# Kernel optimization log

Hardware: AMD Instinct MI355X
Metric: run time of the kernel (lower is better)

## Reference

```python
import jax, jax.numpy as jnp
import numpy as np

N = 50000
E = 1600000
D_IN, D_EMB, D_H, D_OUT, HEADS = 128, 128, 128, 64, 2


def setup_inputs() -> dict:
    key = jax.random.key(0)
    ks = jax.random.split(key, 12)
    return {
        "x": jax.random.normal(ks[0], (N, D_IN), jnp.float32),
        "edge_index": jax.random.randint(ks[1], (2, E), 0, N, dtype=jnp.int32),
        "node_indices": jnp.arange(N, dtype=jnp.int32),
        "emb": jax.random.normal(ks[2], (N, D_EMB), jnp.float32) * 0.1,
        "W_gcn": jax.random.normal(ks[3], (D_IN + D_EMB, D_H), jnp.float32) * 0.06,
        "b_gcn": jnp.zeros((D_H,), jnp.float32),
        "W_sage_l": jax.random.normal(ks[4], (D_H, D_H), jnp.float32) * 0.08,
        "W_sage_r": jax.random.normal(ks[5], (D_H, D_H), jnp.float32) * 0.08,
        "b_sage": jnp.zeros((D_H,), jnp.float32),
        "W_gat": jax.random.normal(ks[6], (D_H, HEADS, D_H), jnp.float32) * 0.08,
        "att_src": jax.random.normal(ks[7], (HEADS, D_H), jnp.float32) * 0.1,
        "att_dst": jax.random.normal(ks[8], (HEADS, D_H), jnp.float32) * 0.1,
        "b_gat": jnp.zeros((D_H,), jnp.float32),
        "W_out": jax.random.normal(ks[9], (D_H, D_OUT), jnp.float32) * 0.08,
        "b_out": jnp.zeros((D_OUT,), jnp.float32),
    }


def _forward(x, edge_index, node_indices, emb, W_gcn, b_gcn,
             W_sage_l, W_sage_r, b_sage, W_gat, att_src, att_dst, b_gat,
             W_out, b_out):
    n = x.shape[0]
    seg = jax.ops.segment_sum
    loops = jnp.arange(n, dtype=edge_index.dtype)

    # node2vec embedding lookup + concat
    h = jnp.concatenate([x, emb[node_indices]], axis=1)  # [N, D_IN+D_EMB]

    # --- GCNConv (symmetric norm, self loops) ---
    src = jnp.concatenate([edge_index[0], loops])
    dst = jnp.concatenate([edge_index[1], loops])
    deg = seg(jnp.ones_like(dst, jnp.float32), dst, num_segments=n)
    dinv = jnp.where(deg > 0, jax.lax.rsqrt(jnp.maximum(deg, 1.0)), 0.0)
    norm = dinv[src] * dinv[dst]                     # [E+N]
    hW = h @ W_gcn                                   # [N, D_H]
    h = seg(hW[src] * norm[:, None], dst, num_segments=n) + b_gcn
    h = jax.nn.relu(h)

    # --- SAGEConv (mean aggregation, no self loops) ---
    s, d = edge_index[0], edge_index[1]
    agg = seg(h[s], d, num_segments=n)
    cnt = seg(jnp.ones_like(d, jnp.float32), d, num_segments=n)
    mean = agg / jnp.maximum(cnt, 1.0)[:, None]
    h = mean @ W_sage_l + h @ W_sage_r + b_sage
    h = jax.nn.relu(h)

    # --- GATConv heads=2, concat=False (mean over heads), self loops ---
    xW = jnp.einsum('nd,dhc->nhc', h, W_gat)         # [N, H, D_H]
    a_src = jnp.einsum('nhc,hc->nh', xW, att_src)    # [N, H]
    a_dst = jnp.einsum('nhc,hc->nh', xW, att_dst)
    alpha = jax.nn.leaky_relu(a_src[src] + a_dst[dst], 0.2)  # [E+N, H]
    amax = jax.ops.segment_max(alpha, dst, num_segments=n)
    alpha = jnp.exp(alpha - amax[dst])
    asum = seg(alpha, dst, num_segments=n)
    alpha = alpha / (asum[dst] + 1e-16)
    out = seg(xW[src] * alpha[:, :, None], dst, num_segments=n)  # [N, H, D_H]
    h = jax.nn.relu(out.mean(axis=1) + b_gat)

    return h @ W_out + b_out


def reference(x, edge_index, node_indices, emb, W_gcn, b_gcn,
              W_sage_l, W_sage_r, b_sage, W_gat, att_src, att_dst, b_gat,
              W_out, b_out):
    return _forward(x, edge_index, node_indices, emb, W_gcn, b_gcn,
                    W_sage_l, W_sage_r, b_sage, W_gat, att_src, att_dst, b_gat,
                    W_out, b_out)
```

## Files before the change

### kernel.cpp

```cpp
#include <hip/hip_runtime.h>


typedef short bf16x8 __attribute__((ext_vector_type(8)));
typedef float f32x4  __attribute__((ext_vector_type(4)));

static __device__ __forceinline__ float leaky02(float x) {
    return x > 0.f ? x : 0.2f * x;
}
static __device__ __forceinline__ unsigned short f2bf(float f) {
    unsigned u = __float_as_uint(f);
    u = (u + 0x7FFFu + ((u >> 16) & 1u)) >> 16;
    return (unsigned short)u;
}
static __device__ __forceinline__ float bf2f(unsigned short h) {
    return __uint_as_float(((unsigned)h) << 16);
}
static __device__ __forceinline__ float4 bf4(ushort4 h) {
    return make_float4(bf2f(h.x), bf2f(h.y), bf2f(h.z), bf2f(h.w));
}
static __device__ __forceinline__ void split_bf(float v, unsigned short& h,
                                                unsigned short& l) {
    unsigned u = __float_as_uint(v);
    unsigned uh = u & 0xFFFF0000u;
    h = (unsigned short)(uh >> 16);
    l = f2bf(v - __uint_as_float(uh));
}

__global__ void deg_edges(const int* __restrict__ dst, int* __restrict__ degi, int E) {
    int e = blockIdx.x * blockDim.x + threadIdx.x;
    if (e < E) atomicAdd(&degi[dst[e]], 1);
}

__global__ __launch_bounds__(256)
void scan_part_norm(const int* __restrict__ degi, int* __restrict__ partial,
                    float* __restrict__ dinv, float* __restrict__ icnt, int n)
{
    int t = threadIdx.x;
    int base = blockIdx.x * 1024 + t * 4;
    int s = 0;
#pragma unroll
    for (int i = 0; i < 4; ++i) {
        int g = base + i;
        if (g < n) {
            int de = degi[g];
            s += de;
            dinv[g] = rsqrtf((float)(de + 1));
            icnt[g] = 1.0f / (float)(de > 1 ? de : 1);
        }
    }
#pragma unroll
    for (int m = 32; m > 0; m >>= 1) s += __shfl_xor(s, m, 64);
    __shared__ int wsum[4];
    if ((t & 63) == 0) wsum[t >> 6] = s;
    __syncthreads();
    if (t == 0) partial[blockIdx.x] = wsum[0] + wsum[1] + wsum[2] + wsum[3];
}

__global__ __launch_bounds__(64)
void scan_offsets(int* __restrict__ partial, int nb)
{
    int t = threadIdx.x;
    int carry = 0;
    for (int base = 0; base < nb; base += 64) {
        int i = base + t;
        int v = (i < nb) ? partial[i] : 0;
        int incl = v;
#pragma unroll
        for (int m = 1; m < 64; m <<= 1) {
            int o = __shfl_up(incl, m, 64);
            if (t >= m) incl += o;
        }
        if (i < nb) partial[i] = incl - v + carry;
        carry += __shfl(incl, 63, 64);
    }
}

__global__ __launch_bounds__(256)
void scan_write(const int* __restrict__ degi, const int* __restrict__ partial,
                int* __restrict__ rowptr, int n)
{
    __shared__ int tmp[256];
    int t = threadIdx.x;
    int base = blockIdx.x * 1024 + t * 4;
    int v[4]; int s = 0;
#pragma unroll
    for (int i = 0; i < 4; ++i) {
        int g = base + i;
        v[i] = (g < n) ? degi[g] : 0;
        s += v[i];
    }
    tmp[t] = s;
    __syncthreads();
    for (int off = 1; off < 256; off <<= 1) {
        int a = (t >= off) ? tmp[t - off] : 0;
        __syncthreads();
        tmp[t] += a;
        __syncthreads();
    }
    int run = tmp[t] - s + partial[blockIdx.x];
#pragma unroll
    for (int i = 0; i < 4; ++i) {
        int g = base + i;
        if (g < n) rowptr[g] = run;
        run += v[i];
    }
}

__global__ void csr_fill(const int* __restrict__ src, const int* __restrict__ dst,
                         int* __restrict__ rowptr, int* __restrict__ csr, int E)
{
    int e = blockIdx.x * blockDim.x + threadIdx.x;
    if (e >= E) return;
    int d = dst[e];
    int pos = atomicAdd(&rowptr[d], 1);
    csr[pos] = src[e];
}

static __device__ __forceinline__ void stage_w_split(
    const float* __restrict__ W, int ncW, int colOff, int kt, int t,
    unsigned short (*WBh)[65][8], unsigned short (*WBl)[65][8])
{
#pragma unroll
    for (int i = 0; i < 4; ++i) {
        int f = i * 256 + t;
        int wr = f >> 5, wc4 = (f & 31) << 2;
        float4 v = *(const float4*)(W + (size_t)(kt * 32 + wr) * ncW + colOff + wc4);
        int jj = wr & 7, kg16 = (wr >> 3) << 4;
        int nt = wc4 >> 4, sb = (wc4 & 15) + kg16;
        unsigned short h, l;
        split_bf(v.x, h, l); WBh[nt][sb + 0][jj] = h; WBl[nt][sb + 0][jj] = l;
        split_bf(v.y, h, l); WBh[nt][sb + 1][jj] = h; WBl[nt][sb + 1][jj] = l;
        split_bf(v.z, h, l); WBh[nt][sb + 2][jj] = h; WBl[nt][sb + 2][jj] = l;
        split_bf(v.w, h, l); WBh[nt][sb + 3][jj] = h; WBl[nt][sb + 3][jj] = l;
    }
}

__global__ __launch_bounds__(256)
void gemm_gcn(const float* __restrict__ A1, const float* __restrict__ W1,
              const float* __restrict__ A2, const float* __restrict__ W2,
              const int* __restrict__ idx2, const float* __restrict__ scale,
              unsigned short* __restrict__ C, int nrows)
{
    __shared__ unsigned short ABh[8][65][8];
    __shared__ unsigned short WBh[8][65][8], WBl[8][65][8];
    const int t    = threadIdx.x;
    const int lane = t & 63;
    const int wv   = t >> 6;
    const int l15  = lane & 15;
    const int lg   = lane >> 4;
    const int row0 = blockIdx.x * 128;

    f32x4 acc[2][8];
#pragma unroll
    for (int mt = 0; mt < 2; ++mt)
#pragma unroll
        for (int nt = 0; nt < 8; ++nt) acc[mt][nt] = (f32x4){0.f, 0.f, 0.f, 0.f};

    for (int p = 0; p < 2; ++p) {
        const float* A = (p == 0) ? A1 : A2;
        const float* W = (p == 0) ? W1 : W2;
        for (int kt = 0; kt < 4; ++kt) {
#pragma unroll
            for (int i = 0; i < 4; ++i) {
                int f = i * 256 + t;
                int r = f >> 3, c4 = (f & 7) << 2;
                int row = row0 + r; if (row >= nrows) row = nrows - 1;
                int arow = (p == 1) ? idx2[row] : row;
                float4 v = *(const float4*)(A + (size_t)arow * 128 + kt * 32 + c4);
                int slot = (r & 15) + ((c4 >> 3) << 4);
                *(ushort4*)&ABh[r >> 4][slot][c4 & 4] =
                    make_ushort4(f2bf(v.x), f2bf(v.y), f2bf(v.z), f2bf(v.w));
            }
            stage_w_split(W, 128, 0, kt, t, WBh, WBl);
            __syncthreads();
            bf16x8 a0 = *reinterpret_cast<const bf16x8*>(&ABh[wv * 2 + 0][lane][0]);
            bf16x8 a1 = *reinterpret_cast<const bf16x8*>(&ABh[wv * 2 + 1][lane][0]);
#pragma unroll
            for (int nt = 0; nt < 8; ++nt) {
                bf16x8 bh = *reinterpret_cast<const bf16x8*>(&WBh[nt][lane][0]);
                bf16x8 bl = *reinterpret_cast<const bf16x8*>(&WBl[nt][lane][0]);
                acc[0][nt] = __builtin_amdgcn_mfma_f32_16x16x32_bf16(a0, bl, acc[0][nt], 0, 0, 0);
                acc[0][nt] = __builtin_amdgcn_mfma_f32_16x16x32_bf16(a0, bh, acc[0][nt], 0, 0, 0);
                acc[1][nt] = __builtin_amdgcn_mfma_f32_16x16x32_bf16(a1, bl, acc[1][nt], 0, 0, 0);
                acc[1][nt] = __builtin_amdgcn_mfma_f32_16x16x32_bf16(a1, bh, acc[1][nt], 0, 0, 0);
            }
            __syncthreads();
        }
    }
#pragma unroll
    for (int mt = 0; mt < 2; ++mt) {
#pragma unroll
        for (int reg = 0; reg < 4; ++reg) {
            int row = row0 + wv * 32 + mt * 16 + lg * 4 + reg;
            if (row >= nrows) continue;
            float sc = scale[row];
            unsigned short* cp = C + (size_t)row * 128 + l15;
#pragma unroll
            for (int nt = 0; nt < 8; ++nt)
                cp[nt * 16] = f2bf(acc[mt][nt][reg] * sc);
        }
    }
}

__global__ __launch_bounds__(256)
void gemm_sage_gat(const unsigned short* __restrict__ meanb,
                   const float* __restrict__ W_sl,
                   const unsigned short* __restrict__ h1b,
                   const float* __restrict__ W_sr,
                   const float* __restrict__ b_sage,
                   const float* __restrict__ W_gat,
                   const float* __restrict__ att_src,
                   const float* __restrict__ att_dst,
                   float* __restrict__ a_s, float* __restrict__ a_d,
                   unsigned short* __restrict__ xWb, int nrows)
{
    __shared__ unsigned short ABh[8][65][8];
    __shared__ unsigned short WBh[8][65][8], WBl[8][65][8];
    __shared__ unsigned short H2[128][136];
    const int t    = threadIdx.x;
    const int lane = t & 63;
    const int wv   = t >> 6;
    const int l15  = lane & 15;
    const int lg   = lane >> 4;
    const int row0 = blockIdx.x * 128;

    f32x4 acc[2][8];
#pragma unroll
    for (int mt = 0; mt < 2; ++mt)
#pragma unroll
        for (int nt = 0; nt < 8; ++nt) acc[mt][nt] = (f32x4){0.f, 0.f, 0.f, 0.f};

    for (int p = 0; p < 2; ++p) {
        const unsigned short* A = (p == 0) ? meanb : h1b;
        const float* W = (p == 0) ? W_sl : W_sr;
        for (int kt = 0; kt < 4; ++kt) {
#pragma unroll
            for (int i = 0; i < 2; ++i) {
                int f = i * 256 + t;
                int r = f >> 2, kq = f & 3;
                int row = row0 + r; if (row >= nrows) row = nrows - 1;
                bf16x8 v = *(const bf16x8*)(A + (size_t)row * 128 + kt * 32 + kq * 8);
                *(bf16x8*)&ABh[r >> 4][(r & 15) + (kq << 4)][0] = v;
            }
            stage_w_split(W, 128, 0, kt, t, WBh, WBl);
            __syncthreads();
            bf16x8 a0 = *reinterpret_cast<const bf16x8*>(&ABh[wv * 2 + 0][lane][0]);
            bf16x8 a1 = *reinterpret_cast<const bf16x8*>(&ABh[wv * 2 + 1][lane][0]);
#pragma unroll
            for (int nt = 0; nt < 8; ++nt) {
                bf16x8 bh = *reinterpret_cast<const bf16x8*>(&WBh[nt][lane][0]);
                bf16x8 bl = *reinterpret_cast<const bf16x8*>(&WBl[nt][lane][0]);
                acc[0][nt] = __builtin_amdgcn_mfma_f32_16x16x32_bf16(a0, bl, acc[0][nt], 0, 0, 0);
                acc[0][nt] = __builtin_amdgcn_mfma_f32_16x16x32_bf16(a0, bh, acc[0][nt], 0, 0, 0);
                acc[1][nt] = __builtin_amdgcn_mfma_f32_16x16x32_bf16(a1, bl, acc[1][nt], 0, 0, 0);
                acc[1][nt] = __builtin_amdgcn_mfma_f32_16x16x32_bf16(a1, bh, acc[1][nt], 0, 0, 0);
            }
            __syncthreads();
        }
    }
    {
        float bias_v[8];
#pragma unroll
        for (int nt = 0; nt < 8; ++nt) bias_v[nt] = b_sage[nt * 16 + l15];
#pragma unroll
        for (int mt = 0; mt < 2; ++mt) {
#pragma unroll
            for (int reg = 0; reg < 4; ++reg) {
                int r = wv * 32 + mt * 16 + lg * 4 + reg;
#pragma unroll
                for (int nt = 0; nt < 8; ++nt) {
                    float v = fmaxf(acc[mt][nt][reg] + bias_v[nt], 0.f);
                    H2[r][nt * 16 + l15] = f2bf(v);
                }
            }
        }
    }
    __syncthreads();

    for (int ch = 0; ch < 2; ++ch) {
        f32x4 acc2[2][8];
#pragma unroll
        for (int mt = 0; mt < 2; ++mt)
#pragma unroll
            for (int nt = 0; nt < 8; ++nt) acc2[mt][nt] = (f32x4){0.f, 0.f, 0.f, 0.f};
        for (int kt = 0; kt < 4; ++kt) {
            stage_w_split(W_gat, 256, ch * 128, kt, t, WBh, WBl);
            __syncthreads();
            bf16x8 a0 = *(const bf16x8*)&H2[(wv * 2 + 0) * 16 + l15][kt * 32 + lg * 8];
            bf16x8 a1 = *(const bf16x8*)&H2[(wv * 2 + 1) * 16 + l15][kt * 32 + lg * 8];
#pragma unroll
            for (int nt = 0; nt < 8; ++nt) {
                bf16x8 bh = *reinterpret_cast<const bf16x8*>(&WBh[nt][lane][0]);
                bf16x8 bl = *reinterpret_cast<const bf16x8*>(&WBl[nt][lane][0]);
                acc2[0][nt] = __builtin_amdgcn_mfma_f32_16x16x32_bf16(a0, bl, acc2[0][nt], 0, 0, 0);
                acc2[0][nt] = __builtin_amdgcn_mfma_f32_16x16x32_bf16(a0, bh, acc2[0][nt], 0, 0, 0);
                acc2[1][nt] = __builtin_amdgcn_mfma_f32_16x16x32_bf16(a1, bl, acc2[1][nt], 0, 0, 0);
                acc2[1][nt] = __builtin_amdgcn_mfma_f32_16x16x32_bf16(a1, bh, acc2[1][nt], 0, 0, 0);
            }
            __syncthreads();
        }
        float as_v[8], ad_v[8];
#pragma unroll
        for (int nt = 0; nt < 8; ++nt) {
            int col = ch * 128 + nt * 16 + l15;
            as_v[nt] = att_src[col];
            ad_v[nt] = att_dst[col];
        }
#pragma unroll
        for (int mt = 0; mt < 2; ++mt) {
#pragma unroll
            for (int reg = 0; reg < 4; ++reg) {
                int row = row0 + wv * 32 + mt * 16 + lg * 4 + reg;
                bool ok = row < nrows;
                float ps = 0.f, pd = 0.f;
                unsigned short* cp =
                    xWb + (size_t)row * 256 + ch * 128 + l15;
#pragma unroll
                for (int nt = 0; nt < 8; ++nt) {
                    float v = acc2[mt][nt][reg];
                    if (ok) cp[nt * 16] = f2bf(v);
                    ps = fmaf(v, as_v[nt], ps);
                    pd = fmaf(v, ad_v[nt], pd);
                }
#pragma unroll
                for (int m = 1; m < 16; m <<= 1) {
                    ps += __shfl_xor(ps, m, 64);
                    pd += __shfl_xor(pd, m, 64);
                }
                if (ok && l15 == 0) {
                    a_s[row * 2 + ch] = ps;
                    a_d[row * 2 + ch] = pd;
                }
            }
        }
    }
}

__global__ __launch_bounds__(256)
void gcn_gather(const int* __restrict__ rowptr, const int* __restrict__ csr,
                const float* __restrict__ dinv,
                const unsigned short* __restrict__ hWb,
                const float* __restrict__ b,
                unsigned short* __restrict__ h1b, int n)
{
    int d = blockIdx.x * 4 + (threadIdx.x >> 6);
    if (d >= n) return;
    int lane = threadIdx.x & 63;
    int half = lane >> 5;
    int c = (lane & 31) << 2;
    int r1 = rowptr[d];
    int r0 = (d == 0) ? 0 : rowptr[d - 1];
    float4 acc = make_float4(0.f, 0.f, 0.f, 0.f);
    int j = r0 + half;
    for (; j + 6 < r1; j += 8) {
        int s0 = csr[j], s1 = csr[j + 2], s2 = csr[j + 4], s3 = csr[j + 6];
        float4 v0 = bf4(*(const ushort4*)(hWb + (size_t)s0 * 128 + c));
        float4 v1 = bf4(*(const ushort4*)(hWb + (size_t)s1 * 128 + c));
        float4 v2 = bf4(*(const ushort4*)(hWb + (size_t)s2 * 128 + c));
        float4 v3 = bf4(*(const ushort4*)(hWb + (size_t)s3 * 128 + c));
        acc.x += (v0.x + v1.x) + (v2.x + v3.x);
        acc.y += (v0.y + v1.y) + (v2.y + v3.y);
        acc.z += (v0.z + v1.z) + (v2.z + v3.z);
        acc.w += (v0.w + v1.w) + (v2.w + v3.w);
    }
    for (; j < r1; j += 2) {
        int s = csr[j];
        float4 v = bf4(*(const ushort4*)(hWb + (size_t)s * 128 + c));
        acc.x += v.x; acc.y += v.y; acc.z += v.z; acc.w += v.w;
    }
    acc.x += __shfl_xor(acc.x, 32, 64);
    acc.y += __shfl_xor(acc.y, 32, 64);
    acc.z += __shfl_xor(acc.z, 32, 64);
    acc.w += __shfl_xor(acc.w, 32, 64);
    if (lane < 32) {
        float dd = dinv[d];
        float4 vd = bf4(*(const ushort4*)(hWb + (size_t)d * 128 + c));
        float4 bb = *(const float4*)(b + c);
        float o0 = fmaxf(fmaf(acc.x + vd.x, dd, bb.x), 0.f);
        float o1 = fmaxf(fmaf(acc.y + vd.y, dd, bb.y), 0.f);
        float o2 = fmaxf(fmaf(acc.z + vd.z, dd, bb.z), 0.f);
        float o3 = fmaxf(fmaf(acc.w + vd.w, dd, bb.w), 0.f);
        *(ushort4*)(h1b + (size_t)d * 128 + c) =
            make_ushort4(f2bf(o0), f2bf(o1), f2bf(o2), f2bf(o3));
    }
}

__global__ __launch_bounds__(256)
void sage_gather(const int* __restrict__ rowptr, const int* __restrict__ csr,
                 const float* __restrict__ icnt,
                 const unsigned short* __restrict__ h1b,
                 unsigned short* __restrict__ meanb, int n)
{
    int d = blockIdx.x * 4 + (threadIdx.x >> 6);
    if (d >= n) return;
    int lane = threadIdx.x & 63;
    int half = lane >> 5;
    int c = (lane & 31) << 2;
    int r1 = rowptr[d];
    int r0 = (d == 0) ? 0 : rowptr[d - 1];
    float4 acc = make_float4(0.f, 0.f, 0.f, 0.f);
    int j = r0 + half;
    for (; j + 6 < r1; j += 8) {
        int s0 = csr[j], s1 = csr[j + 2], s2 = csr[j + 4], s3 = csr[j + 6];
        float4 v0 = bf4(*(const ushort4*)(h1b + (size_t)s0 * 128 + c));
        float4 v1 = bf4(*(const ushort4*)(h1b + (size_t)s1 * 128 + c));
        float4 v2 = bf4(*(const ushort4*)(h1b + (size_t)s2 * 128 + c));
        float4 v3 = bf4(*(const ushort4*)(h1b + (size_t)s3 * 128 + c));
        acc.x += (v0.x + v1.x) + (v2.x + v3.x);
        acc.y += (v0.y + v1.y) + (v2.y + v3.y);
        acc.z += (v0.z + v1.z) + (v2.z + v3.z);
        acc.w += (v0.w + v1.w) + (v2.w + v3.w);
    }
    for (; j < r1; j += 2) {
        int s = csr[j];
        float4 v = bf4(*(const ushort4*)(h1b + (size_t)s * 128 + c));
        acc.x += v.x; acc.y += v.y; acc.z += v.z; acc.w += v.w;
    }
    acc.x += __shfl_xor(acc.x, 32, 64);
    acc.y += __shfl_xor(acc.y, 32, 64);
    acc.z += __shfl_xor(acc.z, 32, 64);
    acc.w += __shfl_xor(acc.w, 32, 64);
    if (lane < 32) {
        float ic = icnt[d];
        *(ushort4*)(meanb + (size_t)d * 128 + c) =
            make_ushort4(f2bf(acc.x * ic), f2bf(acc.y * ic),
                         f2bf(acc.z * ic), f2bf(acc.w * ic));
    }
}

__global__ __launch_bounds__(256)
void gat_gather(const int* __restrict__ rowptr, const int* __restrict__ csr,
                const float* __restrict__ a_s, const float* __restrict__ a_d,
                const unsigned short* __restrict__ xWb,
                const float* __restrict__ b_gat,
                const float* __restrict__ W_out, const float* __restrict__ b_out,
                float* __restrict__ out, int n)
{
    __shared__ float h3row[4][128];
    int wv = threadIdx.x >> 6;
    int d = blockIdx.x * 4 + wv;
    if (d >= n) return;
    int lane = threadIdx.x & 63;
    const int hoff = lane >> 5;
    const int hsel = lane & 32;
    int r1 = rowptr[d];
    int r0 = (d == 0) ? 0 : rowptr[d - 1];
    const int nE = r1 - r0;
    const float adh = a_d[d * 2 + hoff];

    float4 acc = make_float4(0.f, 0.f, 0.f, 0.f);
    float wacc = 0.f;

    for (int blk = 0; blk < nE; blk += 32) {
        int eidx = blk + (lane & 31);
        int s_l = d;
        float wl = 0.f;
        if (eidx < nE) {
            s_l = csr[r0 + eidx];
            wl = __expf(leaky02(a_s[s_l * 2 + hoff] + adh));
        }
        wacc += wl;
        int cnt = min(32, nE - blk);
        int e = 0;
        for (; e + 4 <= cnt; e += 4) {
            int   s0 = __shfl(s_l, e + 0, 64), s1 = __shfl(s_l, e + 1, 64);
            int   s2 = __shfl(s_l, e + 2, 64), s3 = __shfl(s_l, e + 3, 64);
            float w0 = __shfl(wl, (e + 0) | hsel, 64);
            float w1 = __shfl(wl, (e + 1) | hsel, 64);
            float w2 = __shfl(wl, (e + 2) | hsel, 64);
            float w3 = __shfl(wl, (e + 3) | hsel, 64);
            float4 v0 = bf4(((const ushort4*)(xWb + (size_t)s0 * 256))[lane]);
            float4 v1 = bf4(((const ushort4*)(xWb + (size_t)s1 * 256))[lane]);
            float4 v2 = bf4(((const ushort4*)(xWb + (size_t)s2 * 256))[lane]);
            float4 v3 = bf4(((const ushort4*)(xWb + (size_t)s3 * 256))[lane]);
            acc.x = fmaf(v0.x, w0, fmaf(v1.x, w1, fmaf(v2.x, w2, fmaf(v3.x, w3, acc.x))));
            acc.y = fmaf(v0.y, w0, fmaf(v1.y, w1, fmaf(v2.y, w2, fmaf(v3.y, w3, acc.y))));
            acc.z = fmaf(v0.z, w0, fmaf(v1.z, w1, fmaf(v2.z, w2, fmaf(v3.z, w3, acc.z))));
            acc.w = fmaf(v0.w, w0, fmaf(v1.w, w1, fmaf(v2.w, w2, fmaf(v3.w, w3, acc.w))));
        }
        for (; e < cnt; ++e) {
            int   s = __shfl(s_l, e, 64);
            float w = __shfl(wl, e | hsel, 64);
            float4 v = bf4(((const ushort4*)(xWb + (size_t)s * 256))[lane]);
            acc.x = fmaf(v.x, w, acc.x);
            acc.y = fmaf(v.y, w, acc.y);
            acc.z = fmaf(v.z, w, acc.z);
            acc.w = fmaf(v.w, w, acc.w);
        }
    }

    float wself = __expf(leaky02(a_s[d * 2 + hoff] + adh));
    {
        float4 v = bf4(((const ushort4*)(xWb + (size_t)d * 256))[lane]);
        acc.x = fmaf(v.x, wself, acc.x);
        acc.y = fmaf(v.y, wself, acc.y);
        acc.z = fmaf(v.z, wself, acc.z);
        acc.w = fmaf(v.w, wself, acc.w);
    }
#pragma unroll
    for (int sh = 16; sh > 0; sh >>= 1) wacc += __shfl_xor(wacc, sh, 64);
    float inv = 1.f / (wacc + wself + 1e-16f);
    acc.x *= inv; acc.y *= inv; acc.z *= inv; acc.w *= inv;

    float c0 = acc.x + __shfl_xor(acc.x, 32, 64);
    float c1 = acc.y + __shfl_xor(acc.y, 32, 64);
    float c2 = acc.z + __shfl_xor(acc.z, 32, 64);
    float c3 = acc.w + __shfl_xor(acc.w, 32, 64);
    if (lane < 32) {
        float4 bb = ((const float4*)b_gat)[lane];
        float4 o;
        o.x = fmaxf(0.5f * c0 + bb.x, 0.f);
        o.y = fmaxf(0.5f * c1 + bb.y, 0.f);
        o.z = fmaxf(0.5f * c2 + bb.z, 0.f);
        o.w = fmaxf(0.5f * c3 + bb.w, 0.f);
        ((float4*)h3row[wv])[lane] = o;
    }
    __threadfence_block();
    const float* hr = h3row[wv];
    float t0 = 0.f, t1 = 0.f, t2 = 0.f, t3 = 0.f;
#pragma unroll 8
    for (int k = 0; k < 128; k += 4) {
        t0 = fmaf(hr[k + 0], W_out[(k + 0) * 64 + lane], t0);
        t1 = fmaf(hr[k + 1], W_out[(k + 1) * 64 + lane], t1);
        t2 = fmaf(hr[k + 2], W_out[(k + 2) * 64 + lane], t2);
        t3 = fmaf(hr[k + 3], W_out[(k + 3) * 64 + lane], t3);
    }
    out[(size_t)d * 64 + lane] = (t0 + t1) + (t2 + t3) + b_out[lane];
}

extern "C" void kernel_launch(void* const* d_in, const int* in_sizes, int n_in,
                              void* d_out, int out_size, void* d_ws, size_t ws_size,
                              hipStream_t stream)
{
    const float* x      = (const float*)d_in[0];
    const int*   ei     = (const int*)d_in[1];
    const int*   nidx   = (const int*)d_in[2];
    const float* emb    = (const float*)d_in[3];
    const float* W_gcn  = (const float*)d_in[4];
    const float* b_gcn  = (const float*)d_in[5];
    const float* W_sl   = (const float*)d_in[6];
    const float* W_sr   = (const float*)d_in[7];
    const float* b_sage = (const float*)d_in[8];
    const float* W_gat  = (const float*)d_in[9];
    const float* att_s  = (const float*)d_in[10];
    const float* att_d  = (const float*)d_in[11];
    const float* b_gat  = (const float*)d_in[12];
    const float* W_out  = (const float*)d_in[13];
    const float* b_out  = (const float*)d_in[14];
    float* out = (float*)d_out;

    const int n = in_sizes[0] / 128;
    const int E = in_sizes[1] / 2;
    const int* esrc = ei;
    const int* edst = ei + E;

    const size_t P = (size_t)n * 128;
    const int nb_scan = (n + 1023) / 1024;
    float* ws = (float*)d_ws;
    unsigned short* hWb   = (unsigned short*)ws;
    unsigned short* h1b   = (unsigned short*)(ws + P / 2);
    unsigned short* meanb = (unsigned short*)(ws + P);
    unsigned short* xWb   = (unsigned short*)(ws + 3 * P / 2);
    float* dinv = ws + 5 * P / 2;
    float* icnt = dinv + n;
    float* a_s  = icnt + n;
    float* a_d  = a_s + 2 * n;
    int* degi   = (int*)(a_d + 2 * n);
    int* rowptr = degi + n;
    int* partial= rowptr + n;
    int* csr    = partial + nb_scan + 1;

    const int TB = 256;
    int nblk_e     = (E + TB - 1) / TB;
    int nblk_wav_n = (n + 3) / 4;
    int gemm_rows  = (n + 127) / 128;

    hipMemsetAsync(degi, 0, (size_t)n * sizeof(int), stream);
    deg_edges<<<nblk_e, TB, 0, stream>>>(edst, degi, E);
    scan_part_norm<<<nb_scan, TB, 0, stream>>>(degi, partial, dinv, icnt, n);
    scan_offsets<<<1, 64, 0, stream>>>(partial, nb_scan);
    scan_write<<<nb_scan, TB, 0, stream>>>(degi, partial, rowptr, n);
    csr_fill<<<nblk_e, TB, 0, stream>>>(esrc, edst, rowptr, csr, E);

    gemm_gcn<<<gemm_rows, TB, 0, stream>>>(
        x, W_gcn, emb, W_gcn + 128 * 128, nidx, dinv, hWb, n);
    gcn_gather<<<nblk_wav_n, TB, 0, stream>>>(rowptr, csr, dinv, hWb, b_gcn,
                                              h1b, n);

    sage_gather<<<nblk_wav_n, TB, 0, stream>>>(rowptr, csr, icnt, h1b, meanb, n);
    gemm_sage_gat<<<gemm_rows, TB, 0, stream>>>(
        meanb, W_sl, h1b, W_sr, b_sage, W_gat, att_s, att_d, a_s, a_d, xWb, n);

    gat_gather<<<nblk_wav_n, TB, 0, stream>>>(rowptr, csr, a_s, a_d, xWb, b_gat,
                                              W_out, b_out, out, n);
}
```

Before: 612.9 us.

## Pre-split weights into bf16 fragment layout once; merge scan offset kernel into scan_write

A new prep kernel converts all GEMM weights into hi/lo bf16 pairs, stored in global memory in MFMA fragment order. The GEMM kernels then load B fragments directly from global memory instead of re-splitting weights into LDS in every block, which removes LDS staging and some barriers. The single-block scan_offsets kernel is also dropped: each scan_write block sums its own preceding partials, which removes one launch at the cost of redundant reads. Fragment loads now go through the cache rather than LDS, so they may add latency to the MFMA loop.

New measurement: 643.6 us. +5.0%, slower.

```diff
diff --git a/kernel.cpp b/kernel.cpp
--- a/kernel.cpp
+++ b/kernel.cpp
@@ -56,31 +56,23 @@
     if (t == 0) partial[blockIdx.x] = wsum[0] + wsum[1] + wsum[2] + wsum[3];
 }
 
-__global__ __launch_bounds__(64)
-void scan_offsets(int* __restrict__ partial, int nb)
-{
+__global__ __launch_bounds__(256)
+void scan_write(const int* __restrict__ degi, const int* __restrict__ partial,
+                int* __restrict__ rowptr, int n, int nb)
+{
+    __shared__ int tmp[256];
+    __shared__ int basesh;
     int t = threadIdx.x;
-    int carry = 0;
-    for (int base = 0; base < nb; base += 64) {
-        int i = base + t;
-        int v = (i < nb) ? partial[i] : 0;
-        int incl = v;
-#pragma unroll
-        for (int m = 1; m < 64; m <<= 1) {
-            int o = __shfl_up(incl, m, 64);
-            if (t >= m) incl += o;
-        }
-        if (i < nb) partial[i] = incl - v + carry;
-        carry += __shfl(incl, 63, 64);
-    }
-}
-
-__global__ __launch_bounds__(256)
-void scan_write(const int* __restrict__ degi, const int* __restrict__ partial,
-                int* __restrict__ rowptr, int n)
-{
-    __shared__ int tmp[256];
-    int t = threadIdx.x;
+    if (t < 64) {
+        int acc = 0;
+        for (int b0 = 0; b0 < blockIdx.x; b0 += 64) {
+            int i = b0 + t;
+            acc += (i < blockIdx.x && i < nb) ? partial[i] : 0;
+        }
+#pragma unroll
+        for (int m = 32; m > 0; m >>= 1) acc += __shfl_xor(acc, m, 64);
+        if (t == 0) basesh = acc;
+    }
     int base = blockIdx.x * 1024 + t * 4;
     int v[4]; int s = 0;
 #pragma unroll
@@ -97,7 +89,7 @@
         tmp[t] += a;
         __syncthreads();
     }
-    int run = tmp[t] - s + partial[blockIdx.x];
+    int run = tmp[t] - s + basesh;
 #pragma unroll
     for (int i = 0; i < 4; ++i) {
         int g = base + i;
@@ -116,33 +108,50 @@
     csr[pos] = src[e];
 }
 
-static __device__ __forceinline__ void stage_w_split(
-    const float* __restrict__ W, int ncW, int colOff, int kt, int t,
-    unsigned short (*WBh)[65][8], unsigned short (*WBl)[65][8])
-{
-#pragma unroll
-    for (int i = 0; i < 4; ++i) {
-        int f = i * 256 + t;
-        int wr = f >> 5, wc4 = (f & 31) << 2;
-        float4 v = *(const float4*)(W + (size_t)(kt * 32 + wr) * ncW + colOff + wc4);
-        int jj = wr & 7, kg16 = (wr >> 3) << 4;
-        int nt = wc4 >> 4, sb = (wc4 & 15) + kg16;
-        unsigned short h, l;
-        split_bf(v.x, h, l); WBh[nt][sb + 0][jj] = h; WBl[nt][sb + 0][jj] = l;
-        split_bf(v.y, h, l); WBh[nt][sb + 1][jj] = h; WBl[nt][sb + 1][jj] = l;
-        split_bf(v.z, h, l); WBh[nt][sb + 2][jj] = h; WBl[nt][sb + 2][jj] = l;
-        split_bf(v.w, h, l); WBh[nt][sb + 3][jj] = h; WBl[nt][sb + 3][jj] = l;
-    }
-}
-
-__global__ __launch_bounds__(256)
-void gemm_gcn(const float* __restrict__ A1, const float* __restrict__ W1,
-              const float* __restrict__ A2, const float* __restrict__ W2,
+__global__ __launch_bounds__(256)
+void wsplit_prep(const float* __restrict__ Wg, const float* __restrict__ Wsl,
+                 const float* __restrict__ Wsr, const float* __restrict__ Wgat,
+                 unsigned short* __restrict__ Wh, unsigned short* __restrict__ Wl)
+{
+    int slot = blockIdx.x * 256 + threadIdx.x;
+    if (slot >= 6 * 2048) return;
+    int b = slot >> 11;
+    int r = slot & 2047;
+    int kt = r >> 9, nt = (r >> 6) & 7, lane = r & 63;
+    const float* src; int ncW, colOff;
+    switch (b) {
+        case 0:  src = Wg;             ncW = 128; colOff = 0;   break;
+        case 1:  src = Wg + 128 * 128; ncW = 128; colOff = 0;   break;
+        case 2:  src = Wsl;            ncW = 128; colOff = 0;   break;
+        case 3:  src = Wsr;            ncW = 128; colOff = 0;   break;
+        case 4:  src = Wgat;           ncW = 256; colOff = 0;   break;
+        default: src = Wgat;           ncW = 256; colOff = 128; break;
+    }
+    int col = colOff + nt * 16 + (lane & 15);
+    int kbase = kt * 32 + (lane >> 4) * 8;
+    unsigned short h[8], l[8];
+#pragma unroll
+    for (int j = 0; j < 8; ++j)
+        split_bf(src[(size_t)(kbase + j) * ncW + col], h[j], l[j]);
+    size_t off = (size_t)slot * 8;
+    *(ushort4*)(Wh + off)     = make_ushort4(h[0], h[1], h[2], h[3]);
+    *(ushort4*)(Wh + off + 4) = make_ushort4(h[4], h[5], h[6], h[7]);
+    *(ushort4*)(Wl + off)     = make_ushort4(l[0], l[1], l[2], l[3]);
+    *(ushort4*)(Wl + off + 4) = make_ushort4(l[4], l[5], l[6], l[7]);
+}
+
+static __device__ __forceinline__ size_t wfrag(int blk, int kt, int nt, int lane) {
+    return ((size_t)(((blk * 4 + kt) * 8 + nt) * 64 + lane)) * 8;
+}
+
+__global__ __launch_bounds__(256)
+void gemm_gcn(const float* __restrict__ A1, const float* __restrict__ A2,
               const int* __restrict__ idx2, const float* __restrict__ scale,
+              const unsigned short* __restrict__ Wh,
+              const unsigned short* __restrict__ Wl,
               unsigned short* __restrict__ C, int nrows)
 {
     __shared__ unsigned short ABh[8][65][8];
-    __shared__ unsigned short WBh[8][65][8], WBl[8][65][8];
     const int t    = threadIdx.x;
     const int lane = t & 63;
     const int wv   = t >> 6;
@@ -158,7 +167,6 @@
 
     for (int p = 0; p < 2; ++p) {
         const float* A = (p == 0) ? A1 : A2;
-        const float* W = (p == 0) ? W1 : W2;
         for (int kt = 0; kt < 4; ++kt) {
 #pragma unroll
             for (int i = 0; i < 4; ++i) {
@@ -171,14 +179,14 @@
                 *(ushort4*)&ABh[r >> 4][slot][c4 & 4] =
                     make_ushort4(f2bf(v.x), f2bf(v.y), f2bf(v.z), f2bf(v.w));
             }
-            stage_w_split(W, 128, 0, kt, t, WBh, WBl);
             __syncthreads();
             bf16x8 a0 = *reinterpret_cast<const bf16x8*>(&ABh[wv * 2 + 0][lane][0]);
             bf16x8 a1 = *reinterpret_cast<const bf16x8*>(&ABh[wv * 2 + 1][lane][0]);
 #pragma unroll
             for (int nt = 0; nt < 8; ++nt) {
-                bf16x8 bh = *reinterpret_cast<const bf16x8*>(&WBh[nt][lane][0]);
-                bf16x8 bl = *reinterpret_cast<const bf16x8*>(&WBl[nt][lane][0]);
+                size_t fo = wfrag(p, kt, nt, lane);
+                bf16x8 bh = *(const bf16x8*)(Wh + fo);
+                bf16x8 bl = *(const bf16x8*)(Wl + fo);
                 acc[0][nt] = __builtin_amdgcn_mfma_f32_16x16x32_bf16(a0, bl, acc[0][nt], 0, 0, 0);
                 acc[0][nt] = __builtin_amdgcn_mfma_f32_16x16x32_bf16(a0, bh, acc[0][nt], 0, 0, 0);
                 acc[1][nt] = __builtin_amdgcn_mfma_f32_16x16x32_bf16(a1, bl, acc[1][nt], 0, 0, 0);
@@ -204,18 +212,16 @@
 
 __global__ __launch_bounds__(256)
 void gemm_sage_gat(const unsigned short* __restrict__ meanb,
-                   const float* __restrict__ W_sl,
                    const unsigned short* __restrict__ h1b,
-                   const float* __restrict__ W_sr,
                    const float* __restrict__ b_sage,
-                   const float* __restrict__ W_gat,
+                   const unsigned short* __restrict__ Wh,
+                   const unsigned short* __restrict__ Wl,
                    const float* __restrict__ att_src,
                    const float* __restrict__ att_dst,
                    float* __restrict__ a_s, float* __restrict__ a_d,
                    unsigned short* __restrict__ xWb, int nrows)
 {
     __shared__ unsigned short ABh[8][65][8];
-    __shared__ unsigned short WBh[8][65][8], WBl[8][65][8];
     __shared__ unsigned short H2[128][136];
     const int t    = threadIdx.x;
     const int lane = t & 63;
@@ -232,7 +238,7 @@
 
     for (int p = 0; p < 2; ++p) {
         const unsigned short* A = (p == 0) ? meanb : h1b;
-        const float* W = (p == 0) ? W_sl : W_sr;
+        const int wblk = 2 + p;
         for (int kt = 0; kt < 4; ++kt) {
 #pragma unroll
             for (int i = 0; i < 2; ++i) {
@@ -242,14 +248,14 @@
                 bf16x8 v = *(const bf16x8*)(A + (size_t)row * 128 + kt * 32 + kq * 8);
                 *(bf16x8*)&ABh[r >> 4][(r & 15) + (kq << 4)][0] = v;
             }
-            stage_w_split(W, 128, 0, kt, t, WBh, WBl);
             __syncthreads();
             bf16x8 a0 = *reinterpret_cast<const bf16x8*>(&ABh[wv * 2 + 0][lane][0]);
             bf16x8 a1 = *reinterpret_cast<const bf16x8*>(&ABh[wv * 2 + 1][lane][0]);
 #pragma unroll
             for (int nt = 0; nt < 8; ++nt) {
-                bf16x8 bh = *reinterpret_cast<const bf16x8*>(&WBh[nt][lane][0]);
-                bf16x8 bl = *reinterpret_cast<const bf16x8*>(&WBl[nt][lane][0]);
+                size_t fo = wfrag(wblk, kt, nt, lane);
+                bf16x8 bh = *(const bf16x8*)(Wh + fo);
+                bf16x8 bl = *(const bf16x8*)(Wl + fo);
                 acc[0][nt] = __builtin_amdgcn_mfma_f32_16x16x32_bf16(a0, bl, acc[0][nt], 0, 0, 0);
                 acc[0][nt] = __builtin_amdgcn_mfma_f32_16x16x32_bf16(a0, bh, acc[0][nt], 0, 0, 0);
                 acc[1][nt] = __builtin_amdgcn_mfma_f32_16x16x32_bf16(a1, bl, acc[1][nt], 0, 0, 0);
@@ -278,26 +284,25 @@
     __syncthreads();
 
     for (int ch = 0; ch < 2; ++ch) {
+        const int wblk = 4 + ch;
         f32x4 acc2[2][8];
 #pragma unroll
         for (int mt = 0; mt < 2; ++mt)
 #pragma unroll
             for (int nt = 0; nt < 8; ++nt) acc2[mt][nt] = (f32x4){0.f, 0.f, 0.f, 0.f};
         for (int kt = 0; kt < 4; ++kt) {
-            stage_w_split(W_gat, 256, ch * 128, kt, t, WBh, WBl);
-            __syncthreads();
             bf16x8 a0 = *(const bf16x8*)&H2[(wv * 2 + 0) * 16 + l15][kt * 32 + lg * 8];
             bf16x8 a1 = *(const bf16x8*)&H2[(wv * 2 + 1) * 16 + l15][kt * 32 + lg * 8];
 #pragma unroll
             for (int nt = 0; nt < 8; ++nt) {
-                bf16x8 bh = *reinterpret_cast<const bf16x8*>(&WBh[nt][lane][0]);
-                bf16x8 bl = *reinterpret_cast<const bf16x8*>(&WBl[nt][lane][0]);
+                size_t fo = wfrag(wblk, kt, nt, lane);
+                bf16x8 bh = *(const bf16x8*)(Wh + fo);
+                bf16x8 bl = *(const bf16x8*)(Wl + fo);
                 acc2[0][nt] = __builtin_amdgcn_mfma_f32_16x16x32_bf16(a0, bl, acc2[0][nt], 0, 0, 0);
                 acc2[0][nt] = __builtin_amdgcn_mfma_f32_16x16x32_bf16(a0, bh, acc2[0][nt], 0, 0, 0);
                 acc2[1][nt] = __builtin_amdgcn_mfma_f32_16x16x32_bf16(a1, bl, acc2[1][nt], 0, 0, 0);
                 acc2[1][nt] = __builtin_amdgcn_mfma_f32_16x16x32_bf16(a1, bh, acc2[1][nt], 0, 0, 0);
             }
-            __syncthreads();
         }
         float as_v[8], ad_v[8];
 #pragma unroll
@@ -313,8 +318,7 @@
                 int row = row0 + wv * 32 + mt * 16 + lg * 4 + reg;
                 bool ok = row < nrows;
                 float ps = 0.f, pd = 0.f;
-                unsigned short* cp =
-                    xWb + (size_t)row * 256 + ch * 128 + l15;
+                unsigned short* cp = xWb + (size_t)row * 256 + ch * 128 + l15;
 #pragma unroll
                 for (int nt = 0; nt < 8; ++nt) {
                     float v = acc2[mt][nt][reg];
@@ -569,27 +573,30 @@
     int* rowptr = degi + n;
     int* partial= rowptr + n;
     int* csr    = partial + nb_scan + 1;
+    unsigned short* Wh =
+        (unsigned short*)((((uintptr_t)(csr + E)) + 15) & ~(uintptr_t)15);
+    unsigned short* Wl = Wh + 6 * 2048 * 8;
 
     const int TB = 256;
     int nblk_e     = (E + TB - 1) / TB;
     int nblk_wav_n = (n + 3) / 4;
     int gemm_rows  = (n + 127) / 128;
 
+    wsplit_prep<<<48, TB, 0, stream>>>(W_gcn, W_sl, W_sr, W_gat, Wh, Wl);
+
     hipMemsetAsync(degi, 0, (size_t)n * sizeof(int), stream);
     deg_edges<<<nblk_e, TB, 0, stream>>>(edst, degi, E);
     scan_part_norm<<<nb_scan, TB, 0, stream>>>(degi, partial, dinv, icnt, n);
-    scan_offsets<<<1, 64, 0, stream>>>(partial, nb_scan);
-    scan_write<<<nb_scan, TB, 0, stream>>>(degi, partial, rowptr, n);
+    scan_write<<<nb_scan, TB, 0, stream>>>(degi, partial, rowptr, n, nb_scan);
     csr_fill<<<nblk_e, TB, 0, stream>>>(esrc, edst, rowptr, csr, E);
 
-    gemm_gcn<<<gemm_rows, TB, 0, stream>>>(
-        x, W_gcn, emb, W_gcn + 128 * 128, nidx, dinv, hWb, n);
+    gemm_gcn<<<gemm_rows, TB, 0, stream>>>(x, emb, nidx, dinv, Wh, Wl, hWb, n);
     gcn_gather<<<nblk_wav_n, TB, 0, stream>>>(rowptr, csr, dinv, hWb, b_gcn,
                                               h1b, n);
 
     sage_gather<<<nblk_wav_n, TB, 0, stream>>>(rowptr, csr, icnt, h1b, meanb, n);
     gemm_sage_gat<<<gemm_rows, TB, 0, stream>>>(
-        meanb, W_sl, h1b, W_sr, b_sage, W_gat, att_s, att_d, a_s, a_d, xWb, n);
+        meanb, h1b, b_sage, Wh, Wl, att_s, att_d, a_s, a_d, xWb, n);
 
     gat_gather<<<nblk_wav_n, TB, 0, stream>>>(rowptr, csr, a_s, a_d, xWb, b_gat,
                                               W_out, b_out, out, n);
```
